# Kernel optimization log

Hardware: AMD Instinct MI355X
Metric: run time of the kernel (lower is better)

Reference implementation:

```python
import jax, jax.numpy as jnp
import numpy as np

EMBED_DIM = 1024
T1, T2, B = 2048, 2048, 4


def setup_inputs() -> dict:
    key = jax.random.key(0)
    ks = jax.random.split(key, 11)
    s = 1.0 / np.sqrt(EMBED_DIM)
    inp = {
        "x1": jax.random.normal(ks[0], (T1, B, EMBED_DIM), jnp.float32),
        "x2": jax.random.normal(ks[1], (T2, B, EMBED_DIM), jnp.float32),
        "x3": jax.random.normal(ks[2], (T2, B, EMBED_DIM), jnp.float32),
        "wq": jax.random.normal(ks[3], (EMBED_DIM, EMBED_DIM), jnp.float32) * s,
        "bq": jnp.zeros((EMBED_DIM,), jnp.float32),
        "wk": jax.random.normal(ks[4], (EMBED_DIM, EMBED_DIM), jnp.float32) * s,
        "bk": jnp.zeros((EMBED_DIM,), jnp.float32),
        "wv": jax.random.normal(ks[5], (EMBED_DIM, EMBED_DIM), jnp.float32) * s,
        "bv": jnp.zeros((EMBED_DIM,), jnp.float32),
        "wu": jax.random.normal(ks[6], (EMBED_DIM, EMBED_DIM), jnp.float32) * s,
        "bu": jnp.zeros((EMBED_DIM,), jnp.float32),
    }
    return inp


def reference(x1, x2, x3, wq, bq, wk, bk, wv, bv, wu, bu):
    # x1: [T1,B,C], x2: [T2,B,C]; x3 is unused by the original forward.
    C = x1.shape[-1]
    x1b = jnp.swapaxes(x1, 0, 1)  # [B,T1,C]
    x2b = jnp.swapaxes(x2, 0, 1)  # [B,T2,C]
    q = x1b @ wq.T + bq           # [B,T1,C]
    k = x2b @ wk.T + bk           # [B,T2,C]
    v = x2b @ wv.T + bv           # [B,T2,C]
    # single-head attention over full embed dim (num_heads unused in forward)
    scores = jnp.einsum("btc,bsc->bts", q, k) / jnp.sqrt(jnp.float32(C))
    attn = jax.nn.softmax(scores, axis=-1)  # [B,T1,T2]
    # dropout omitted (eval mode / deterministic reference)
    x = jnp.einsum("bts,bsc->btc", attn, v)  # [B,T1,C]
    x = x @ wu.T + bu
    return jnp.swapaxes(x, 0, 1)  # [T1,B,C]
```

## Files before the change

### kernel.cpp

```cpp
#include <hip/hip_runtime.h>
#include <hip/hip_bf16.h>
#include <stdint.h>

#define T1 2048
#define T2 2048
#define NB 4
#define CC 1024

typedef __attribute__((ext_vector_type(4))) float   f32x4;
typedef __attribute__((ext_vector_type(8))) __bf16  bf16x8;
typedef __attribute__((ext_vector_type(8))) unsigned short u16x8;

__device__ __forceinline__ unsigned short f2bf(float f) {
    union { float f; uint32_t u; } x; x.f = f;
    uint32_t u = x.u;
    uint32_t r = (u + 0x7fffu + ((u >> 16) & 1u)) >> 16;
    return (unsigned short)r;
}

__device__ __forceinline__ float bf2f(unsigned short b) {
    return __uint_as_float(((uint32_t)b) << 16);
}

__device__ __forceinline__ void gll16(const void* g, void* l) {
    __builtin_amdgcn_global_load_lds((const __attribute__((address_space(1))) void*)g,
                                     (__attribute__((address_space(3))) void*)l, 16, 0, 0);
}

__global__ __launch_bounds__(256) void convall_k(const float* __restrict__ wq,
                                                 const float* __restrict__ wk,
                                                 const float* __restrict__ wv,
                                                 const float* __restrict__ wu,
                                                 const float* __restrict__ x1,
                                                 const float* __restrict__ x2,
                                                 unsigned short* __restrict__ dst) {
    size_t idx = ((size_t)blockIdx.x * 256 + threadIdx.x) * 8;
    const float* s;
    size_t off;
    if (idx < 4194304) {
        int wsel = (int)(idx >> 20);
        s = (wsel == 0) ? wq : (wsel == 1) ? wk : (wsel == 2) ? wv : wu;
        off = idx & 1048575;
    } else if (idx < 12582912) {
        s = x1; off = idx - 4194304;
    } else {
        s = x2; off = idx - 12582912;
    }
    f32x4 a = *(const f32x4*)(s + off);
    f32x4 b = *(const f32x4*)(s + off + 4);
    u16x8 o;
    o[0] = f2bf(a.x); o[1] = f2bf(a.y); o[2] = f2bf(a.z); o[3] = f2bf(a.w);
    o[4] = f2bf(b.x); o[5] = f2bf(b.y); o[6] = f2bf(b.z); o[7] = f2bf(b.w);
    *(u16x8*)(dst + idx) = o;
}

enum { M_PROJQ = 0, M_PROJK, M_PROJV, M_SCORES, M_PV, M_OUT };

template <int MODE, int KDIM>
__global__ __launch_bounds__(256) void gemm_bt(const unsigned short* __restrict__ Aptr,
                                               const unsigned short* __restrict__ Bptr,
                                               const float* __restrict__ bias,
                                               void* __restrict__ Out) {
    __shared__ unsigned short As[128 * 32];
    __shared__ unsigned short Bs[128 * 32];

    const int tid  = threadIdx.x;
    const int lane = tid & 63;
    const int w    = tid >> 6;
    const int wr   = w >> 1, wc = w & 1;
    const int m0   = blockIdx.y * 128;
    const int n0   = blockIdx.x * 128;
    const int z    = blockIdx.z;

    size_t aoff = 0, boff = 0;
    if constexpr (MODE == M_SCORES) { aoff = (size_t)z * T1 * CC; boff = (size_t)z * T2 * CC; }
    if constexpr (MODE == M_PV)     { aoff = (size_t)z * T1 * T2; boff = (size_t)z * CC * T2; }

    const unsigned short* Ab = Aptr + aoff;
    const unsigned short* Bb = Bptr + boff;

    f32x4 acc[4][4] = {};

    const int ln15 = lane & 15;
    const int l4   = lane >> 4;
    const int srow = tid >> 2, sseg = tid & 3;

    for (int kt = 0; kt < KDIM; kt += 32) {
        __syncthreads();
#pragma unroll
        for (int p = 0; p < 2; ++p) {
            int c = p * 256 + tid;
            int row = p * 64 + srow;
            gll16(Ab + (size_t)(m0 + row) * KDIM + kt + sseg * 8, &As[c * 8]);
        }
#pragma unroll
        for (int p = 0; p < 2; ++p) {
            int c = p * 256 + tid;
            int row = p * 64 + srow;
            gll16(Bb + (size_t)(n0 + row) * KDIM + kt + sseg * 8, &Bs[c * 8]);
        }
        __syncthreads();
        bf16x8 af[4], bf[4];
#pragma unroll
        for (int i = 0; i < 4; ++i) {
            int arow = wr * 64 + i * 16 + ln15;
            af[i] = *(const bf16x8*)(&As[arow * 32 + l4 * 8]);
            int brow = wc * 64 + i * 16 + ln15;
            bf[i] = *(const bf16x8*)(&Bs[brow * 32 + l4 * 8]);
        }
#pragma unroll
        for (int i = 0; i < 4; ++i)
#pragma unroll
            for (int j = 0; j < 4; ++j)
                acc[i][j] = __builtin_amdgcn_mfma_f32_16x16x32_bf16(af[i], bf[j], acc[i][j], 0, 0, 0);
    }

#pragma unroll
    for (int j = 0; j < 4; ++j) {
        const int n = n0 + wc * 64 + j * 16 + ln15;
        float bval = 0.f;
        if constexpr (MODE == M_PROJQ || MODE == M_PROJK || MODE == M_PROJV || MODE == M_OUT)
            bval = bias[n];
#pragma unroll
        for (int i = 0; i < 4; ++i) {
#pragma unroll
            for (int r = 0; r < 4; ++r) {
                const int m = m0 + wr * 64 + i * 16 + l4 * 4 + r;
                float val = acc[i][j][r];
                if constexpr (MODE == M_PROJQ || MODE == M_PROJK) {
                    unsigned short* o = (unsigned short*)Out;
                    o[(size_t)(m & 3) * (T1 * CC) + (size_t)(m >> 2) * CC + n] = f2bf(val + bval);
                } else if constexpr (MODE == M_PROJV) {
                    unsigned short* o = (unsigned short*)Out;
                    o[(size_t)(m & 3) * (CC * T2) + (size_t)n * T2 + (m >> 2)] = f2bf(val + bval);
                } else if constexpr (MODE == M_SCORES) {
                    unsigned short* o = (unsigned short*)Out + (size_t)z * T1 * T2;
                    o[(size_t)m * T2 + n] = f2bf(val * 0.03125f);
                } else if constexpr (MODE == M_PV) {
                    unsigned short* o = (unsigned short*)Out + (size_t)z * T1 * CC;
                    o[(size_t)m * CC + n] = f2bf(val);
                } else {
                    float* o = (float*)Out;
                    o[(size_t)(m & (T1 - 1)) * (NB * CC) + (size_t)(m >> 11) * CC + n] = val + bval;
                }
            }
        }
    }
}

__global__ __launch_bounds__(256) void softmax_k(unsigned short* __restrict__ SP) {
    const int tid = threadIdx.x, lane = tid & 63, w = tid >> 6;
    unsigned short* p = SP + (size_t)blockIdx.x * T2;
    u16x8 v = *(const u16x8*)(p + tid * 8);
    float f[8];
#pragma unroll
    for (int j = 0; j < 8; ++j) f[j] = bf2f(v[j]);
    float mx = f[0];
#pragma unroll
    for (int j = 1; j < 8; ++j) mx = fmaxf(mx, f[j]);
#pragma unroll
    for (int off = 32; off; off >>= 1) mx = fmaxf(mx, __shfl_xor(mx, off));
    __shared__ float red[8];
    if (lane == 0) red[w] = mx;
    __syncthreads();
    mx = fmaxf(fmaxf(red[0], red[1]), fmaxf(red[2], red[3]));
    float s = 0.f, e[8];
#pragma unroll
    for (int j = 0; j < 8; ++j) { e[j] = __expf(f[j] - mx); s += e[j]; }
#pragma unroll
    for (int off = 32; off; off >>= 1) s += __shfl_xor(s, off);
    if (lane == 0) red[4 + w] = s;
    __syncthreads();
    s = red[4] + red[5] + red[6] + red[7];
    float inv = 1.f / s;
    u16x8 o;
#pragma unroll
    for (int j = 0; j < 8; ++j) o[j] = f2bf(e[j] * inv);
    *(u16x8*)(p + tid * 8) = o;
}

extern "C" void kernel_launch(void* const* d_in, const int* in_sizes, int n_in,
                              void* d_out, int out_size, void* d_ws, size_t ws_size,
                              hipStream_t stream) {
    const float* x1 = (const float*)d_in[0];
    const float* x2 = (const float*)d_in[1];
    const float* wq = (const float*)d_in[3];
    const float* bq = (const float*)d_in[4];
    const float* wk = (const float*)d_in[5];
    const float* bk = (const float*)d_in[6];
    const float* wv = (const float*)d_in[7];
    const float* bv = (const float*)d_in[8];
    const float* wu = (const float*)d_in[9];
    const float* bu = (const float*)d_in[10];

    char* ws = (char*)d_ws;
    const size_t WB_OFF  = 0;
    const size_t XB1_OFF = 8388608;
    const size_t XB2_OFF = 25165824;
    const size_t SP_OFF  = 8388608;
    const size_t Q_OFF   = 41943040;
    const size_t K_OFF   = 58720256;
    const size_t V_OFF   = 75497472;
    const size_t O_OFF   = 41943040;
    const size_t WS_END  = 92274688;
    if (ws_size < WS_END) return;

    unsigned short* wb  = (unsigned short*)(ws + WB_OFF);
    unsigned short* Xb1 = (unsigned short*)(ws + XB1_OFF);
    unsigned short* Xb2 = (unsigned short*)(ws + XB2_OFF);
    unsigned short* SP  = (unsigned short*)(ws + SP_OFF);
    unsigned short* Qb  = (unsigned short*)(ws + Q_OFF);
    unsigned short* Kb  = (unsigned short*)(ws + K_OFF);
    unsigned short* Vt  = (unsigned short*)(ws + V_OFF);
    unsigned short* Ob  = (unsigned short*)(ws + O_OFF);

    convall_k<<<dim3(10240), 256, 0, stream>>>(wq, wk, wv, wu, x1, x2, wb);

    gemm_bt<M_PROJQ, 1024><<<dim3(8, 64, 1), 256, 0, stream>>>(Xb1, wb,               bq, Qb);
    gemm_bt<M_PROJK, 1024><<<dim3(8, 64, 1), 256, 0, stream>>>(Xb2, wb + 1048576,     bk, Kb);
    gemm_bt<M_PROJV, 1024><<<dim3(8, 64, 1), 256, 0, stream>>>(Xb2, wb + 2 * 1048576, bv, Vt);

    gemm_bt<M_SCORES, 1024><<<dim3(16, 16, 4), 256, 0, stream>>>(Qb, Kb, nullptr, SP);

    softmax_k<<<dim3(8192), 256, 0, stream>>>(SP);

    gemm_bt<M_PV, 2048><<<dim3(8, 16, 4), 256, 0, stream>>>(SP, Vt, nullptr, Ob);

    gemm_bt<M_OUT, 1024><<<dim3(8, 64, 1), 256, 0, stream>>>(Ob, wb + 3 * 1048576, bu, d_out);
}
```

Before: 400.0 us.

## Fuse K/V projections and remap GEMM blocks for per-XCD L2 locality

Merges the K and V projection GEMMs into a single N=2048 GEMM that writes K row-major and V transposed, sharing reads of the converted x2. All GEMM launches switch to a 1D grid with an explicit block-to-tile mapping that groups tiles sharing A rows (and batch) on the same XCD, aiming to improve L2 hit rates. Adds a per-element branch in the KV epilogue and extra kernel arguments.

```diff
diff --git a/kernel.cpp b/kernel.cpp
--- a/kernel.cpp
+++ b/kernel.cpp
@@ -54,13 +54,15 @@
     *(u16x8*)(dst + idx) = o;
 }
 
-enum { M_PROJQ = 0, M_PROJK, M_PROJV, M_SCORES, M_PV, M_OUT };
+enum { M_PROJQ = 0, M_KV, M_SCORES, M_PV, M_OUT };
 
 template <int MODE, int KDIM>
 __global__ __launch_bounds__(256) void gemm_bt(const unsigned short* __restrict__ Aptr,
                                                const unsigned short* __restrict__ Bptr,
                                                const float* __restrict__ bias,
-                                               void* __restrict__ Out) {
+                                               const float* __restrict__ bias2,
+                                               void* __restrict__ Out,
+                                               void* __restrict__ Out2) {
     __shared__ unsigned short As[128 * 32];
     __shared__ unsigned short Bs[128 * 32];
 
@@ -68,9 +70,32 @@
     const int lane = tid & 63;
     const int w    = tid >> 6;
     const int wr   = w >> 1, wc = w & 1;
-    const int m0   = blockIdx.y * 128;
-    const int n0   = blockIdx.x * 128;
-    const int z    = blockIdx.z;
+
+    const int bid = blockIdx.x;
+    const int xcd = bid & 7;
+    const int i   = bid >> 3;
+    int m0, n0, z = 0;
+    if constexpr (MODE == M_SCORES) {
+        z = xcd >> 1;
+        const int mhalf = xcd & 1;
+        const int nblk = i >> 3, mloc = i & 7;
+        m0 = (mhalf * 8 + mloc) * 128;
+        n0 = nblk * 128;
+    } else if constexpr (MODE == M_PV) {
+        z = xcd >> 1;
+        const int nhalf = xcd & 1;
+        const int nloc = i & 3, mblk = i >> 2;
+        m0 = mblk * 128;
+        n0 = (nhalf * 4 + nloc) * 128;
+    } else if constexpr (MODE == M_KV) {
+        const int mloc = i & 7, nblk = i >> 3;
+        m0 = (xcd * 8 + mloc) * 128;
+        n0 = nblk * 128;
+    } else {
+        const int mloc = i & 7, nblk = i >> 3;
+        m0 = (xcd * 8 + mloc) * 128;
+        n0 = nblk * 128;
+    }
 
     size_t aoff = 0, boff = 0;
     if constexpr (MODE == M_SCORES) { aoff = (size_t)z * T1 * CC; boff = (size_t)z * T2 * CC; }
@@ -102,37 +127,44 @@
         __syncthreads();
         bf16x8 af[4], bf[4];
 #pragma unroll
-        for (int i = 0; i < 4; ++i) {
-            int arow = wr * 64 + i * 16 + ln15;
-            af[i] = *(const bf16x8*)(&As[arow * 32 + l4 * 8]);
-            int brow = wc * 64 + i * 16 + ln15;
-            bf[i] = *(const bf16x8*)(&Bs[brow * 32 + l4 * 8]);
-        }
-#pragma unroll
-        for (int i = 0; i < 4; ++i)
+        for (int i2 = 0; i2 < 4; ++i2) {
+            int arow = wr * 64 + i2 * 16 + ln15;
+            af[i2] = *(const bf16x8*)(&As[arow * 32 + l4 * 8]);
+            int brow = wc * 64 + i2 * 16 + ln15;
+            bf[i2] = *(const bf16x8*)(&Bs[brow * 32 + l4 * 8]);
+        }
+#pragma unroll
+        for (int i2 = 0; i2 < 4; ++i2)
 #pragma unroll
             for (int j = 0; j < 4; ++j)
-                acc[i][j] = __builtin_amdgcn_mfma_f32_16x16x32_bf16(af[i], bf[j], acc[i][j], 0, 0, 0);
+                acc[i2][j] = __builtin_amdgcn_mfma_f32_16x16x32_bf16(af[i2], bf[j], acc[i2][j], 0, 0, 0);
     }
 
 #pragma unroll
     for (int j = 0; j < 4; ++j) {
         const int n = n0 + wc * 64 + j * 16 + ln15;
         float bval = 0.f;
-        if constexpr (MODE == M_PROJQ || MODE == M_PROJK || MODE == M_PROJV || MODE == M_OUT)
+        if constexpr (MODE == M_PROJQ || MODE == M_OUT)
             bval = bias[n];
-#pragma unroll
-        for (int i = 0; i < 4; ++i) {
+        if constexpr (MODE == M_KV)
+            bval = (n < CC) ? bias[n] : bias2[n - CC];
+#pragma unroll
+        for (int i2 = 0; i2 < 4; ++i2) {
 #pragma unroll
             for (int r = 0; r < 4; ++r) {
-                const int m = m0 + wr * 64 + i * 16 + l4 * 4 + r;
-                float val = acc[i][j][r];
-                if constexpr (MODE == M_PROJQ || MODE == M_PROJK) {
+                const int m = m0 + wr * 64 + i2 * 16 + l4 * 4 + r;
+                float val = acc[i2][j][r];
+                if constexpr (MODE == M_PROJQ) {
                     unsigned short* o = (unsigned short*)Out;
                     o[(size_t)(m & 3) * (T1 * CC) + (size_t)(m >> 2) * CC + n] = f2bf(val + bval);
-                } else if constexpr (MODE == M_PROJV) {
-                    unsigned short* o = (unsigned short*)Out;
-                    o[(size_t)(m & 3) * (CC * T2) + (size_t)n * T2 + (m >> 2)] = f2bf(val + bval);
+                } else if constexpr (MODE == M_KV) {
+                    if (n < CC) {
+                        unsigned short* o = (unsigned short*)Out;
+                        o[(size_t)(m & 3) * (T2 * CC) + (size_t)(m >> 2) * CC + n] = f2bf(val + bval);
+                    } else {
+                        unsigned short* o = (unsigned short*)Out2;
+                        o[(size_t)(m & 3) * (CC * T2) + (size_t)(n - CC) * T2 + (m >> 2)] = f2bf(val + bval);
+                    }
                 } else if constexpr (MODE == M_SCORES) {
                     unsigned short* o = (unsigned short*)Out + (size_t)z * T1 * T2;
                     o[(size_t)m * T2 + n] = f2bf(val * 0.03125f);
@@ -216,15 +248,15 @@
 
     convall_k<<<dim3(10240), 256, 0, stream>>>(wq, wk, wv, wu, x1, x2, wb);
 
-    gemm_bt<M_PROJQ, 1024><<<dim3(8, 64, 1), 256, 0, stream>>>(Xb1, wb,               bq, Qb);
-    gemm_bt<M_PROJK, 1024><<<dim3(8, 64, 1), 256, 0, stream>>>(Xb2, wb + 1048576,     bk, Kb);
-    gemm_bt<M_PROJV, 1024><<<dim3(8, 64, 1), 256, 0, stream>>>(Xb2, wb + 2 * 1048576, bv, Vt);
-
-    gemm_bt<M_SCORES, 1024><<<dim3(16, 16, 4), 256, 0, stream>>>(Qb, Kb, nullptr, SP);
+    gemm_bt<M_PROJQ, 1024><<<dim3(512), 256, 0, stream>>>(Xb1, wb, bq, nullptr, Qb, nullptr);
+
+    gemm_bt<M_KV, 1024><<<dim3(1024), 256, 0, stream>>>(Xb2, wb + 1048576, bk, bv, Kb, Vt);
+
+    gemm_bt<M_SCORES, 1024><<<dim3(1024), 256, 0, stream>>>(Qb, Kb, nullptr, nullptr, SP, nullptr);
 
     softmax_k<<<dim3(8192), 256, 0, stream>>>(SP);
 
-    gemm_bt<M_PV, 2048><<<dim3(8, 16, 4), 256, 0, stream>>>(SP, Vt, nullptr, Ob);
-
-    gemm_bt<M_OUT, 1024><<<dim3(8, 64, 1), 256, 0, stream>>>(Ob, wb + 3 * 1048576, bu, d_out);
-}
+    gemm_bt<M_PV, 2048><<<dim3(512), 256, 0, stream>>>(SP, Vt, nullptr, nullptr, Ob, nullptr);
+
+    gemm_bt<M_OUT, 1024><<<dim3(512), 256, 0, stream>>>(Ob, wb + 3 * 1048576, bu, nullptr, d_out, nullptr);
+}
```

New measurement: 374.3 us. -6.4%, faster.
